# Optimization experiments

Measured on AMD Instinct MI355X. Metric: run time of the kernel, lower is better.

## Reference

```python
import jax, jax.numpy as jnp
import numpy as np

B, S, D, H = 4, 2048, 1024, 4096
EPS = 1e-5

def _layernorm(x, g, b):
    mu = jnp.mean(x, axis=-1, keepdims=True)
    var = jnp.mean(jnp.square(x - mu), axis=-1, keepdims=True)
    return (x - mu) * jax.lax.rsqrt(var + EPS) * g + b

def setup_inputs() -> dict:
    key = jax.random.key(0)
    ks = jax.random.split(key, 8)
    s = lambda d: 1.0 / np.sqrt(d)
    return {
        "x": jax.random.normal(ks[0], (B, S, D), jnp.float32),
        "Wq": jax.random.normal(ks[1], (D, D), jnp.float32) * s(D),
        "bq": jnp.zeros((D,), jnp.float32),
        "Wk": jax.random.normal(ks[2], (D, D), jnp.float32) * s(D),
        "bk": jnp.zeros((D,), jnp.float32),
        "Wv": jax.random.normal(ks[3], (D, D), jnp.float32) * s(D),
        "bv": jnp.zeros((D,), jnp.float32),
        "Wo": jax.random.normal(ks[4], (D, D), jnp.float32) * s(D),
        "bo": jnp.zeros((D,), jnp.float32),
        "g1": jnp.ones((D,), jnp.float32),
        "be1": jnp.zeros((D,), jnp.float32),
        "g2": jnp.ones((D,), jnp.float32),
        "be2": jnp.zeros((D,), jnp.float32),
        "W1": jax.random.normal(ks[5], (D, H), jnp.float32) * s(D),
        "b1": jnp.zeros((H,), jnp.float32),
        "W2": jax.random.normal(ks[6], (H, D), jnp.float32) * s(H),
        "b2": jnp.zeros((D,), jnp.float32),
    }

def reference(x, Wq, bq, Wk, bk, Wv, bv, Wo, bo, g1, be1, g2, be2, W1, b1, W2, b2):
    # pre-norm self-attention + residual
    xn = _layernorm(x, g1, be1)
    q = xn @ Wq + bq            # [B,S,D]
    k = xn @ Wk + bk
    v = xn @ Wv + bv
    scale = 1.0 / jnp.sqrt(jnp.float32(D))
    scores = jnp.einsum("bsd,btd->bst", q, k) * scale  # [B,S,S]
    attn = jax.nn.softmax(scores, axis=-1)
    attn_out = jnp.einsum("bst,btd->bsd", attn, v) @ Wo + bo
    x = x + attn_out
    # pre-norm MLP + residual
    xn2 = _layernorm(x, g2, be2)
    ffn = jax.nn.relu(xn2 @ W1 + b1) @ W2 + b2
    out = x + ffn
    return out, attn
```

## Files before the change

### kernel.cpp

```cpp
#include <hip/hip_runtime.h>
#include <hip/hip_bf16.h>


typedef __bf16 bf16_t;
typedef __bf16 bf16x8 __attribute__((ext_vector_type(8)));
typedef float  f32x4  __attribute__((ext_vector_type(4)));

#define EPI_QKV            0
#define EPI_F32_SCALE      2
#define EPI_BF16           3
#define EPI_F32_BIAS_RES   4
#define EPI_BF16_RELU_BIAS 5

__device__ __forceinline__ void gl_lds16(const bf16_t* g, void* l) {
  __builtin_amdgcn_global_load_lds(
      (const __attribute__((address_space(1))) void*)g,
      (__attribute__((address_space(3))) void*)l, 16, 0, 0);
}

template<int BM, int EPI>
__global__ __launch_bounds__(512, 2)
void gemm8p(const bf16_t* __restrict__ A, const bf16_t* __restrict__ B,
            float* __restrict__ Cf, bf16_t* __restrict__ Cb,
            bf16_t* __restrict__ Cb2, bf16_t* __restrict__ Cb3,
            const float* __restrict__ bias, const float* __restrict__ bias2,
            const float* __restrict__ bias3,
            int M, int N, int K, long sAb, long sBb, long sCb, float scale)
{
  constexpr int BN  = 256;
  constexpr int WTM = BM / 2;
  constexpr int MF  = WTM / 16;
  constexpr int NF  = 4;
  constexpr int LA  = BM / 128;
  constexpr int LB  = 2;
  constexpr int L   = LA + LB;
  constexpr int L0  = 2;
  constexpr int SBUF = (BM + BN) * 64;
  constexpr int W   = 2 * L;
  __shared__ __align__(16) char lds[4 * SBUF];

  const int tid = threadIdx.x;
  const int l   = tid & 63;
  const int w   = tid >> 6;
  const int wm  = w >> 2;
  const int wn  = w & 3;

  const int nx = gridDim.x, ny = gridDim.y;
  const int tot = nx * ny * gridDim.z;
  int id = blockIdx.x + nx * (blockIdx.y + ny * blockIdx.z);
  const int cpx = tot >> 3;
  int s = (id & 7) * cpx + (id >> 3);
  const int bx = s % nx; int rq = s / nx;
  const int by = rq % ny; const int bz = rq / ny;

  const bf16_t* Ab = A + (long)bz * sAb;
  const bf16_t* Bb = B + (long)bz * sBb;
  const int m0 = by * BM, n0 = bx * BN;
  const int NT = K >> 5;

  const int srow = w * 16 + (l >> 2);
  const int scol = ((l & 3) ^ ((l >> 3) & 3)) * 8;
  const bf16_t* srcA[LA]; const bf16_t* srcB[LB];
#pragma unroll
  for (int q = 0; q < LA; ++q) srcA[q] = Ab + (long)(m0 + q * 128 + srow) * K + scol;
#pragma unroll
  for (int q = 0; q < LB; ++q) srcB[q] = Bb + (long)(n0 + q * 128 + srow) * K + scol;
  const int ldsA = w * 1024;
  const int ldsB = BM * 64 + w * 1024;

  const int rA0 = wm * WTM + (l & 15);
  const int rB0 = wn * 64 + (l & 15);
  const int xoff = 16 * ((l >> 4) ^ ((l >> 1) & 3));

  f32x4 acc[MF][NF] = {};
  bf16x8 afr[MF / 2], bfr[NF];

#pragma unroll
  for (int d = 0; d < 3; ++d) {
    char* bufS = lds + d * SBUF;
    const long kst = (long)d * 32;
#pragma unroll
    for (int q = 0; q < LA; ++q) gl_lds16(srcA[q] + kst, bufS + ldsA + q * 8192);
#pragma unroll
    for (int q = 0; q < LB; ++q) gl_lds16(srcB[q] + kst, bufS + ldsB + q * 8192);
  }
  asm volatile("s_waitcnt vmcnt(%0)" :: "n"(W) : "memory");
  __builtin_amdgcn_s_barrier();
  __builtin_amdgcn_sched_barrier(0);

  for (int t = 0; t < NT; ++t) {
    const char* bufR = lds + (t & 3) * SBUF;
    char* bufS = lds + ((t + 3) & 3) * SBUF;
    const int tst = t + 3;
    const long kst = (long)((tst < NT) ? tst : (NT - 1)) * 32;

#pragma unroll
    for (int nf = 0; nf < NF; ++nf)
      bfr[nf] = *(const bf16x8*)(bufR + BM * 64 + (rB0 + nf * 16) * 64 + xoff);
#pragma unroll
    for (int mf = 0; mf < MF / 2; ++mf)
      afr[mf] = *(const bf16x8*)(bufR + (rA0 + mf * 16) * 64 + xoff);
#pragma unroll
    for (int q = 0; q < L0; ++q) {
      if (q < LA) gl_lds16(srcA[q] + kst, bufS + ldsA + q * 8192);
      else        gl_lds16(srcB[q - LA] + kst, bufS + ldsB + (q - LA) * 8192);
    }
    __builtin_amdgcn_s_barrier();
    __builtin_amdgcn_s_setprio(1);
#pragma unroll
    for (int mf = 0; mf < MF / 2; ++mf)
#pragma unroll
      for (int nf = 0; nf < NF; ++nf)
        acc[mf][nf] = __builtin_amdgcn_mfma_f32_16x16x32_bf16(afr[mf], bfr[nf], acc[mf][nf], 0, 0, 0);
    __builtin_amdgcn_s_setprio(0);
    __builtin_amdgcn_s_barrier();

#pragma unroll
    for (int mf = 0; mf < MF / 2; ++mf)
      afr[mf] = *(const bf16x8*)(bufR + (rA0 + (MF / 2 + mf) * 16) * 64 + xoff);
#pragma unroll
    for (int q = L0; q < L; ++q) {
      if (q < LA) gl_lds16(srcA[q] + kst, bufS + ldsA + q * 8192);
      else        gl_lds16(srcB[q - LA] + kst, bufS + ldsB + (q - LA) * 8192);
    }
    __builtin_amdgcn_s_barrier();
    __builtin_amdgcn_s_setprio(1);
#pragma unroll
    for (int mf = 0; mf < MF / 2; ++mf)
#pragma unroll
      for (int nf = 0; nf < NF; ++nf)
        acc[MF / 2 + mf][nf] = __builtin_amdgcn_mfma_f32_16x16x32_bf16(afr[mf], bfr[nf], acc[MF / 2 + mf][nf], 0, 0, 0);
    __builtin_amdgcn_s_setprio(0);
    asm volatile("s_waitcnt vmcnt(%0)" :: "n"(W) : "memory");
    __builtin_amdgcn_s_barrier();
    __builtin_amdgcn_sched_barrier(0);
  }
  asm volatile("s_waitcnt vmcnt(0)" ::: "memory");

  const int colB0 = n0 + wn * 64 + (l & 15);
  const int rowB0 = m0 + wm * WTM + ((l >> 4) << 2);
#pragma unroll
  for (int mi = 0; mi < MF; ++mi) {
#pragma unroll
    for (int ni = 0; ni < NF; ++ni) {
      const int col = colB0 + ni * 16;
#pragma unroll
      for (int j = 0; j < 4; ++j) {
        const int row = rowB0 + mi * 16 + j;
        const float v = acc[mi][ni][j];
        if constexpr (EPI == EPI_F32_SCALE) {
          Cf[sCb * bz + (long)row * N + col] = v * scale;
        } else if constexpr (EPI == EPI_QKV) {
          if (col < 1024)      Cb [(long)row * 1024 + col]        = (bf16_t)(v + bias[col]);
          else if (col < 2048) Cb2[(long)row * 1024 + col - 1024] = (bf16_t)(v + bias2[col - 1024]);
          else                 Cb3[(long)row * 1024 + col - 2048] = (bf16_t)(v + bias3[col - 2048]);
        } else {
          const float u = v + bias[col];
          Cb[(long)row * N + col] = (bf16_t)(u > 0.f ? u : 0.f);
        }
      }
    }
  }
}

template<int EPI>
__global__ __launch_bounds__(512, 1)
void gemm128(const bf16_t* __restrict__ A, const bf16_t* __restrict__ B,
             float* __restrict__ Cf, bf16_t* __restrict__ Cb,
             const float* __restrict__ bias, const float* __restrict__ resid,
             int M, int N, int K, long sAb, long sBb, long sCb)
{
  constexpr int SBUF = 49152;
  __shared__ __align__(16) char lds[3 * SBUF];
  const int tid = threadIdx.x;
  const int l   = tid & 63;
  const int w   = tid >> 6;
  const int wm  = w >> 2, wn = w & 3;

  const int nx = gridDim.x, ny = gridDim.y;
  const int tot = nx * ny * gridDim.z;
  int id = blockIdx.x + nx * (blockIdx.y + ny * blockIdx.z);
  const int cpx = tot >> 3;
  int sid = (id & 7) * cpx + (id >> 3);
  const int bx = sid % nx; int rq = sid / nx;
  const int by = rq % ny; const int bz = rq / ny;

  const bf16_t* Ab = A + (long)bz * sAb;
  const bf16_t* Bb = B + (long)bz * sBb;
  const int m0 = by * 128, n0 = bx * 256;
  const int NT = K >> 6;

  const int scol = ((l & 7) ^ (l >> 3)) * 8;
  const bf16_t* srcA = Ab + (long)(m0 + 16 * w + (l >> 3)) * K + scol;
  const bf16_t* srcB = Bb + (long)(n0 + 32 * w + (l >> 3)) * K + scol;
  const int dA = w * 2048 + l * 16;
  const int dB = 16384 + w * 4096 + l * 16;

  const int rA = wm * 64 + (l & 15);
  const int rB = wn * 64 + (l & 15);
  const int xo = ((l >> 4) ^ (l & 7)) * 16;
  const int aoff = rA * 128 + xo;
  const int boff = 16384 + rB * 128 + xo;

  f32x4 acc[4][4] = {};
  bf16x8 af[4], bv[4];

  {
    char* b0 = lds; char* b1 = lds + SBUF;
#pragma unroll
    for (int q = 0; q < 2; ++q) gl_lds16(srcA + (long)q * 8 * K, b0 + dA + q * 1024);
#pragma unroll
    for (int q = 0; q < 4; ++q) gl_lds16(srcB + (long)q * 8 * K, b0 + dB + q * 1024);
#pragma unroll
    for (int q = 0; q < 2; ++q) gl_lds16(srcA + (long)q * 8 * K + 64, b1 + dA + q * 1024);
#pragma unroll
    for (int q = 0; q < 4; ++q) gl_lds16(srcB + (long)q * 8 * K + 64, b1 + dB + q * 1024);
  }
  asm volatile("s_waitcnt vmcnt(6)" ::: "memory");
  __builtin_amdgcn_s_barrier();
  __builtin_amdgcn_sched_barrier(0);

  int ir = 0, is = 2;
  for (int t = 0; t < NT; ++t) {
    const char* bufR = lds + ir * SBUF;
    char* bufS = lds + is * SBUF;
    const int tst = (t + 2 < NT) ? t + 2 : NT - 1;
    const long kst = (long)tst * 64;

#pragma unroll
    for (int nf = 0; nf < 4; ++nf) bv[nf] = *(const bf16x8*)(bufR + boff + nf * 2048);
#pragma unroll
    for (int mf = 0; mf < 4; ++mf) af[mf] = *(const bf16x8*)(bufR + aoff + mf * 2048);
    gl_lds16(srcA + kst,                 bufS + dA);
    gl_lds16(srcA + (long)8 * K + kst,   bufS + dA + 1024);
    gl_lds16(srcB + kst,                 bufS + dB);
    __builtin_amdgcn_s_barrier();
    __builtin_amdgcn_s_setprio(1);
#pragma unroll
    for (int mf = 0; mf < 4; ++mf)
#pragma unroll
      for (int nf = 0; nf < 4; ++nf)
        acc[mf][nf] = __builtin_amdgcn_mfma_f32_16x16x32_bf16(af[mf], bv[nf], acc[mf][nf], 0, 0, 0);
    __builtin_amdgcn_s_setprio(0);
    __builtin_amdgcn_s_barrier();

#pragma unroll
    for (int nf = 0; nf < 4; ++nf) bv[nf] = *(const bf16x8*)(bufR + ((boff + nf * 2048) ^ 64));
#pragma unroll
    for (int mf = 0; mf < 4; ++mf) af[mf] = *(const bf16x8*)(bufR + ((aoff + mf * 2048) ^ 64));
    gl_lds16(srcB + (long)8 * K + kst,   bufS + dB + 1024);
    gl_lds16(srcB + (long)16 * K + kst,  bufS + dB + 2048);
    gl_lds16(srcB + (long)24 * K + kst,  bufS + dB + 3072);
    __builtin_amdgcn_s_barrier();
    __builtin_amdgcn_s_setprio(1);
#pragma unroll
    for (int mf = 0; mf < 4; ++mf)
#pragma unroll
      for (int nf = 0; nf < 4; ++nf)
        acc[mf][nf] = __builtin_amdgcn_mfma_f32_16x16x32_bf16(af[mf], bv[nf], acc[mf][nf], 0, 0, 0);
    __builtin_amdgcn_s_setprio(0);
    asm volatile("s_waitcnt vmcnt(6)" ::: "memory");
    __builtin_amdgcn_s_barrier();
    __builtin_amdgcn_sched_barrier(0);
    ir = (ir == 2) ? 0 : ir + 1;
    is = (is == 2) ? 0 : is + 1;
  }
  asm volatile("s_waitcnt vmcnt(0)" ::: "memory");

  const int colB0 = n0 + wn * 64 + (l & 15);
  const int rowB0 = m0 + wm * 64 + ((l >> 4) << 2);
#pragma unroll
  for (int mi = 0; mi < 4; ++mi) {
#pragma unroll
    for (int ni = 0; ni < 4; ++ni) {
      const int col = colB0 + ni * 16;
#pragma unroll
      for (int j = 0; j < 4; ++j) {
        const int row = rowB0 + mi * 16 + j;
        const float v = acc[mi][ni][j];
        if constexpr (EPI == EPI_BF16) {
          Cb[sCb * bz + (long)row * N + col] = (bf16_t)v;
        } else {
          Cf[(long)row * N + col] = v + bias[col] + resid[(long)row * N + col];
        }
      }
    }
  }
}

__global__ __launch_bounds__(256)
void transpose_bf(const bf16_t* __restrict__ V, bf16_t* __restrict__ VT)
{
  __shared__ __align__(16) bf16_t t[64][72];
  const int b = blockIdx.z;
  const int t0 = blockIdx.y * 64, d0 = blockIdx.x * 64;
  const int r = threadIdx.x >> 3;
  const int c = (threadIdx.x & 7) * 8;
  const bf16_t* src = V + ((long)b * 2048 + t0) * 1024 + d0;
#pragma unroll
  for (int h = 0; h < 2; ++h)
    *(bf16x8*)&t[r + 32 * h][c] = *(const bf16x8*)(src + (long)(r + 32 * h) * 1024 + c);
  __syncthreads();
  bf16_t* dst = VT + ((long)b * 1024 + d0) * 2048 + t0;
#pragma unroll
  for (int h = 0; h < 2; ++h) {
    const int d = r + 32 * h;
    bf16x8 o;
#pragma unroll
    for (int j = 0; j < 8; ++j) o[j] = t[c + j][d];
    *(bf16x8*)(dst + (long)d * 2048 + c) = o;
  }
}

__global__ __launch_bounds__(256)
void ln_kernel(const float* __restrict__ x, const float* __restrict__ g,
               const float* __restrict__ be, bf16_t* __restrict__ out)
{
  const long row = blockIdx.x;
  const float4 v = *(const float4*)(x + row * 1024 + threadIdx.x * 4);
  float s  = v.x + v.y + v.z + v.w;
  float s2 = v.x * v.x + v.y * v.y + v.z * v.z + v.w * v.w;
  __shared__ float red[10];
  const int lane = threadIdx.x & 63, w = threadIdx.x >> 6;
#pragma unroll
  for (int off = 32; off; off >>= 1) {
    s  += __shfl_down(s, off);
    s2 += __shfl_down(s2, off);
  }
  if (lane == 0) { red[w] = s; red[4 + w] = s2; }
  __syncthreads();
  if (threadIdx.x == 0) {
    const float ts = red[0] + red[1] + red[2] + red[3];
    const float t2 = red[4] + red[5] + red[6] + red[7];
    const float mu = ts * (1.f / 1024.f);
    const float var = t2 * (1.f / 1024.f) - mu * mu;
    red[8] = mu;
    red[9] = rsqrtf(var + 1e-5f);
  }
  __syncthreads();
  const float mu = red[8], rinv = red[9];
  const int c = threadIdx.x * 4;
  const float4 gv = *(const float4*)(g + c);
  const float4 bvv = *(const float4*)(be + c);
  bf16_t* o = out + row * 1024 + c;
  o[0] = (bf16_t)((v.x - mu) * rinv * gv.x + bvv.x);
  o[1] = (bf16_t)((v.y - mu) * rinv * gv.y + bvv.y);
  o[2] = (bf16_t)((v.z - mu) * rinv * gv.z + bvv.z);
  o[3] = (bf16_t)((v.w - mu) * rinv * gv.w + bvv.w);
}

__global__ __launch_bounds__(256)
void softmax_kernel(float* __restrict__ sc, bf16_t* __restrict__ ab)
{
  const long row = blockIdx.x;
  float* sr = sc + row * 2048;
  const int t0 = threadIdx.x * 8;
  const float4 a = *(const float4*)(sr + t0);
  const float4 b = *(const float4*)(sr + t0 + 4);
  float mx = fmaxf(fmaxf(fmaxf(a.x, a.y), fmaxf(a.z, a.w)),
                   fmaxf(fmaxf(b.x, b.y), fmaxf(b.z, b.w)));
  __shared__ float red[4];
  __shared__ float bc[2];
  const int lane = threadIdx.x & 63, w = threadIdx.x >> 6;
#pragma unroll
  for (int off = 32; off; off >>= 1) mx = fmaxf(mx, __shfl_down(mx, off));
  if (lane == 0) red[w] = mx;
  __syncthreads();
  if (threadIdx.x == 0) bc[0] = fmaxf(fmaxf(red[0], red[1]), fmaxf(red[2], red[3]));
  __syncthreads();
  const float m = bc[0];
  float e[8];
  e[0] = __expf(a.x - m); e[1] = __expf(a.y - m); e[2] = __expf(a.z - m); e[3] = __expf(a.w - m);
  e[4] = __expf(b.x - m); e[5] = __expf(b.y - m); e[6] = __expf(b.z - m); e[7] = __expf(b.w - m);
  float s = e[0] + e[1] + e[2] + e[3] + e[4] + e[5] + e[6] + e[7];
#pragma unroll
  for (int off = 32; off; off >>= 1) s += __shfl_down(s, off);
  __syncthreads();
  if (lane == 0) red[w] = s;
  __syncthreads();
  if (threadIdx.x == 0) bc[1] = 1.f / (red[0] + red[1] + red[2] + red[3]);
  __syncthreads();
  const float inv = bc[1];
  float4 oa, ob;
  oa.x = e[0] * inv; oa.y = e[1] * inv; oa.z = e[2] * inv; oa.w = e[3] * inv;
  ob.x = e[4] * inv; ob.y = e[5] * inv; ob.z = e[6] * inv; ob.w = e[7] * inv;
  *(float4*)(sr + t0)     = oa;
  *(float4*)(sr + t0 + 4) = ob;
  bf16x8 o8;
  o8[0] = (bf16_t)oa.x; o8[1] = (bf16_t)oa.y; o8[2] = (bf16_t)oa.z; o8[3] = (bf16_t)oa.w;
  o8[4] = (bf16_t)ob.x; o8[5] = (bf16_t)ob.y; o8[6] = (bf16_t)ob.z; o8[7] = (bf16_t)ob.w;
  *(bf16x8*)(ab + row * 2048 + t0) = o8;
}

__global__ __launch_bounds__(256)
void transpose_cvt(const float* __restrict__ W, bf16_t* __restrict__ WT, int R, int C)
{
  __shared__ float t[32][33];
  const int c0 = blockIdx.x * 32, r0 = blockIdx.y * 32;
  const int tx = threadIdx.x & 31, ty = threadIdx.x >> 5;
#pragma unroll
  for (int i = 0; i < 32; i += 8)
    t[ty + i][tx] = W[(long)(r0 + ty + i) * C + c0 + tx];
  __syncthreads();
#pragma unroll
  for (int i = 0; i < 32; i += 8)
    WT[(long)(c0 + ty + i) * R + r0 + tx] = (bf16_t)t[tx][ty + i];
}

extern "C" void kernel_launch(void* const* d_in, const int* in_sizes, int n_in,
                              void* d_out, int out_size, void* d_ws, size_t ws_size,
                              hipStream_t stream)
{
  const float* x   = (const float*)d_in[0];
  const float* Wq  = (const float*)d_in[1];
  const float* bq  = (const float*)d_in[2];
  const float* Wk  = (const float*)d_in[3];
  const float* bk  = (const float*)d_in[4];
  const float* Wv  = (const float*)d_in[5];
  const float* bv  = (const float*)d_in[6];
  const float* Wo  = (const float*)d_in[7];
  const float* bo  = (const float*)d_in[8];
  const float* g1  = (const float*)d_in[9];
  const float* be1 = (const float*)d_in[10];
  const float* g2  = (const float*)d_in[11];
  const float* be2 = (const float*)d_in[12];
  const float* W1  = (const float*)d_in[13];
  const float* b1  = (const float*)d_in[14];
  const float* W2  = (const float*)d_in[15];
  const float* b2  = (const float*)d_in[16];

  float* out   = (float*)d_out;
  float* attnF = out + 8192L * 1024;
  bf16_t* vB   = (bf16_t*)attnF;

  char* ws = (char*)d_ws;
  const size_t MB = 1024 * 1024;
  bf16_t* WqkvT = (bf16_t*)(ws + 0 * MB);
  bf16_t* WoT   = (bf16_t*)(ws + 6 * MB);
  bf16_t* W1T   = (bf16_t*)(ws + 8 * MB);
  bf16_t* W2T   = (bf16_t*)(ws + 16 * MB);
  bf16_t* xn    = (bf16_t*)(ws + 24 * MB);
  bf16_t* qB    = (bf16_t*)(ws + 40 * MB);
  bf16_t* kB    = (bf16_t*)(ws + 56 * MB);
  bf16_t* vT    = (bf16_t*)(ws + 72 * MB);
  bf16_t* atB   = (bf16_t*)(ws + 88 * MB);
  float*  x2    = (float* )(ws + 120 * MB);
  bf16_t* hB    = (bf16_t*)(ws + 56 * MB);

  transpose_cvt<<<dim3(32, 32),  256, 0, stream>>>(Wq, WqkvT,                1024, 1024);
  transpose_cvt<<<dim3(32, 32),  256, 0, stream>>>(Wk, WqkvT + 1024L * 1024, 1024, 1024);
  transpose_cvt<<<dim3(32, 32),  256, 0, stream>>>(Wv, WqkvT + 2048L * 1024, 1024, 1024);
  transpose_cvt<<<dim3(32, 32),  256, 0, stream>>>(Wo, WoT, 1024, 1024);
  transpose_cvt<<<dim3(128, 32), 256, 0, stream>>>(W1, W1T, 1024, 4096);
  transpose_cvt<<<dim3(32, 128), 256, 0, stream>>>(W2, W2T, 4096, 1024);

  ln_kernel<<<8192, 256, 0, stream>>>(x, g1, be1, xn);

  gemm8p<256, EPI_QKV><<<dim3(12, 32, 1), 512, 0, stream>>>(
      xn, WqkvT, nullptr, qB, kB, vB, bq, bk, bv,
      8192, 3072, 1024, 0, 0, 0, 1.f);

  transpose_bf<<<dim3(16, 32, 4), 256, 0, stream>>>(vB, vT);

  gemm8p<256, EPI_F32_SCALE><<<dim3(8, 8, 4), 512, 0, stream>>>(
      qB, kB, attnF, nullptr, nullptr, nullptr, nullptr, nullptr, nullptr,
      2048, 2048, 1024, 2048L * 1024, 2048L * 1024, 2048L * 2048, 0.03125f);

  softmax_kernel<<<8192, 256, 0, stream>>>(attnF, atB);

  gemm128<EPI_BF16><<<dim3(4, 16, 4), 512, 0, stream>>>(
      atB, vT, nullptr, qB, nullptr, nullptr,
      2048, 1024, 2048, 2048L * 2048, 1024L * 2048, 2048L * 1024);

  gemm128<EPI_F32_BIAS_RES><<<dim3(4, 64, 1), 512, 0, stream>>>(
      qB, WoT, x2, nullptr, bo, x,
      8192, 1024, 1024, 0, 0, 0);

  ln_kernel<<<8192, 256, 0, stream>>>(x2, g2, be2, xn);

  gemm8p<256, EPI_BF16_RELU_BIAS><<<dim3(16, 32, 1), 512, 0, stream>>>(
      xn, W1T, nullptr, hB, nullptr, nullptr, b1, nullptr, nullptr,
      8192, 4096, 1024, 0, 0, 0, 1.f);
  gemm128<EPI_F32_BIAS_RES><<<dim3(4, 64, 1), 512, 0, stream>>>(
      hB, W2T, out, nullptr, b2, x2,
      8192, 1024, 4096, 0, 0, 0);
}
```

Measured before the change: 428.1 us.

## Store attention scores as bf16 and add a dedicated 128x256 QKV GEMM

The scores GEMM now writes scaled logits as bf16 into the bf16 attention buffer instead of fp32 into the fp32 attention output. Softmax reads those bf16 logits, then writes the fp32 probabilities and overwrites the bf16 copy in place. This cuts the scores write and the softmax read traffic roughly in half. The QKV projection moves to a new simpler double-buffered 128x256 tile kernel with K-step 32 and 2 blocks per CU, for better occupancy. The cost is that logits are rounded to bf16 before softmax, which reduces accuracy of the returned attention matrix.

```diff
diff --git a/kernel.cpp b/kernel.cpp
--- a/kernel.cpp
+++ b/kernel.cpp
@@ -7,7 +7,7 @@
 typedef float  f32x4  __attribute__((ext_vector_type(4)));
 
 #define EPI_QKV            0
-#define EPI_F32_SCALE      2
+#define EPI_BF16_SCALE     1
 #define EPI_BF16           3
 #define EPI_F32_BIAS_RES   4
 #define EPI_BF16_RELU_BIAS 5
@@ -22,9 +22,7 @@
 __global__ __launch_bounds__(512, 2)
 void gemm8p(const bf16_t* __restrict__ A, const bf16_t* __restrict__ B,
             float* __restrict__ Cf, bf16_t* __restrict__ Cb,
-            bf16_t* __restrict__ Cb2, bf16_t* __restrict__ Cb3,
-            const float* __restrict__ bias, const float* __restrict__ bias2,
-            const float* __restrict__ bias3,
+            const float* __restrict__ bias,
             int M, int N, int K, long sAb, long sBb, long sCb, float scale)
 {
   constexpr int BN  = 256;
@@ -148,12 +146,8 @@
       for (int j = 0; j < 4; ++j) {
         const int row = rowB0 + mi * 16 + j;
         const float v = acc[mi][ni][j];
-        if constexpr (EPI == EPI_F32_SCALE) {
-          Cf[sCb * bz + (long)row * N + col] = v * scale;
-        } else if constexpr (EPI == EPI_QKV) {
-          if (col < 1024)      Cb [(long)row * 1024 + col]        = (bf16_t)(v + bias[col]);
-          else if (col < 2048) Cb2[(long)row * 1024 + col - 1024] = (bf16_t)(v + bias2[col - 1024]);
-          else                 Cb3[(long)row * 1024 + col - 2048] = (bf16_t)(v + bias3[col - 2048]);
+        if constexpr (EPI == EPI_BF16_SCALE) {
+          Cb[sCb * bz + (long)row * N + col] = (bf16_t)(v * scale);
         } else {
           const float u = v + bias[col];
           Cb[(long)row * N + col] = (bf16_t)(u > 0.f ? u : 0.f);
@@ -288,6 +282,98 @@
   }
 }
 
+__global__ __launch_bounds__(512, 2)
+void gemm128_32(const bf16_t* __restrict__ A, const bf16_t* __restrict__ B,
+                bf16_t* __restrict__ Cb, bf16_t* __restrict__ Cb2,
+                bf16_t* __restrict__ Cb3,
+                const float* __restrict__ bias, const float* __restrict__ bias2,
+                const float* __restrict__ bias3, int M, int N, int K)
+{
+  constexpr int SBUF = 24576;
+  __shared__ __align__(16) char lds[2 * SBUF];
+  const int tid = threadIdx.x;
+  const int l   = tid & 63;
+  const int w   = tid >> 6;
+  const int wm  = w >> 2, wn = w & 3;
+
+  const int nx = gridDim.x, ny = gridDim.y;
+  const int tot = nx * ny;
+  int id = blockIdx.x + nx * blockIdx.y;
+  const int cpx = tot >> 3;
+  int sid = (id & 7) * cpx + (id >> 3);
+  const int bx = sid % nx;
+  const int by = sid / nx;
+
+  const int m0 = by * 128, n0 = bx * 256;
+  const int NT = K >> 5;
+
+  const int srow = (l >> 2);
+  const int scol = ((l & 3) ^ ((l >> 3) & 3)) * 8;
+  const bf16_t* srcA = A + (long)(m0 + w * 16 + srow) * K + scol;
+  const bf16_t* srcB0 = B + (long)(n0 + w * 32 + srow) * K + scol;
+  const bf16_t* srcB1 = srcB0 + (long)16 * K;
+  const int dA = w * 1024 + l * 16;
+  const int dB = 8192 + w * 2048 + l * 16;
+
+  const int rA = wm * 64 + (l & 15);
+  const int rB = wn * 64 + (l & 15);
+  const int xoff = 16 * ((l >> 4) ^ ((l >> 1) & 3));
+  const int aoff = rA * 64 + xoff;
+  const int boff = 8192 + rB * 64 + xoff;
+
+  f32x4 acc[4][4] = {};
+  bf16x8 af[4], bv[4];
+
+  gl_lds16(srcA, lds + dA);
+  gl_lds16(srcB0, lds + dB);
+  gl_lds16(srcB1, lds + dB + 1024);
+  asm volatile("s_waitcnt vmcnt(0)" ::: "memory");
+  __builtin_amdgcn_s_barrier();
+  __builtin_amdgcn_sched_barrier(0);
+
+  for (int t = 0; t < NT; ++t) {
+    const char* bufR = lds + (t & 1) * SBUF;
+    char* bufS = lds + ((t + 1) & 1) * SBUF;
+    const long kst = (long)((t + 1 < NT) ? t + 1 : NT - 1) * 32;
+
+#pragma unroll
+    for (int nf = 0; nf < 4; ++nf) bv[nf] = *(const bf16x8*)(bufR + boff + nf * 1024);
+#pragma unroll
+    for (int mf = 0; mf < 4; ++mf) af[mf] = *(const bf16x8*)(bufR + aoff + mf * 1024);
+    gl_lds16(srcA + kst, bufS + dA);
+    gl_lds16(srcB0 + kst, bufS + dB);
+    gl_lds16(srcB1 + kst, bufS + dB + 1024);
+    __builtin_amdgcn_s_setprio(1);
+#pragma unroll
+    for (int mf = 0; mf < 4; ++mf)
+#pragma unroll
+      for (int nf = 0; nf < 4; ++nf)
+        acc[mf][nf] = __builtin_amdgcn_mfma_f32_16x16x32_bf16(af[mf], bv[nf], acc[mf][nf], 0, 0, 0);
+    __builtin_amdgcn_s_setprio(0);
+    asm volatile("s_waitcnt vmcnt(0)" ::: "memory");
+    __builtin_amdgcn_s_barrier();
+    __builtin_amdgcn_sched_barrier(0);
+  }
+
+  const int colB0 = n0 + wn * 64 + (l & 15);
+  const int rowB0 = m0 + wm * 64 + ((l >> 4) << 2);
+#pragma unroll
+  for (int mi = 0; mi < 4; ++mi) {
+#pragma unroll
+    for (int ni = 0; ni < 4; ++ni) {
+      const int col = colB0 + ni * 16;
+#pragma unroll
+      for (int j = 0; j < 4; ++j) {
+        const int row = rowB0 + mi * 16 + j;
+        const float v = acc[mi][ni][j];
+        if (col < 1024)      Cb [(long)row * 1024 + col]        = (bf16_t)(v + bias[col]);
+        else if (col < 2048) Cb2[(long)row * 1024 + col - 1024] = (bf16_t)(v + bias2[col - 1024]);
+        else                 Cb3[(long)row * 1024 + col - 2048] = (bf16_t)(v + bias3[col - 2048]);
+      }
+    }
+  }
+}
+
 __global__ __launch_bounds__(256)
 void transpose_bf(const bf16_t* __restrict__ V, bf16_t* __restrict__ VT)
 {
@@ -353,12 +439,13 @@
 void softmax_kernel(float* __restrict__ sc, bf16_t* __restrict__ ab)
 {
   const long row = blockIdx.x;
-  float* sr = sc + row * 2048;
   const int t0 = threadIdx.x * 8;
-  const float4 a = *(const float4*)(sr + t0);
-  const float4 b = *(const float4*)(sr + t0 + 4);
-  float mx = fmaxf(fmaxf(fmaxf(a.x, a.y), fmaxf(a.z, a.w)),
-                   fmaxf(fmaxf(b.x, b.y), fmaxf(b.z, b.w)));
+  const bf16x8 v8 = *(const bf16x8*)(ab + row * 2048 + t0);
+  float e[8];
+#pragma unroll
+  for (int j = 0; j < 8; ++j) e[j] = (float)v8[j];
+  float mx = fmaxf(fmaxf(fmaxf(e[0], e[1]), fmaxf(e[2], e[3])),
+                   fmaxf(fmaxf(e[4], e[5]), fmaxf(e[6], e[7])));
   __shared__ float red[4];
   __shared__ float bc[2];
   const int lane = threadIdx.x & 63, w = threadIdx.x >> 6;
@@ -369,10 +456,9 @@
   if (threadIdx.x == 0) bc[0] = fmaxf(fmaxf(red[0], red[1]), fmaxf(red[2], red[3]));
   __syncthreads();
   const float m = bc[0];
-  float e[8];
-  e[0] = __expf(a.x - m); e[1] = __expf(a.y - m); e[2] = __expf(a.z - m); e[3] = __expf(a.w - m);
-  e[4] = __expf(b.x - m); e[5] = __expf(b.y - m); e[6] = __expf(b.z - m); e[7] = __expf(b.w - m);
-  float s = e[0] + e[1] + e[2] + e[3] + e[4] + e[5] + e[6] + e[7];
+  float s = 0.f;
+#pragma unroll
+  for (int j = 0; j < 8; ++j) { e[j] = __expf(e[j] - m); s += e[j]; }
 #pragma unroll
   for (int off = 32; off; off >>= 1) s += __shfl_down(s, off);
   __syncthreads();
@@ -384,8 +470,8 @@
   float4 oa, ob;
   oa.x = e[0] * inv; oa.y = e[1] * inv; oa.z = e[2] * inv; oa.w = e[3] * inv;
   ob.x = e[4] * inv; ob.y = e[5] * inv; ob.z = e[6] * inv; ob.w = e[7] * inv;
-  *(float4*)(sr + t0)     = oa;
-  *(float4*)(sr + t0 + 4) = ob;
+  *(float4*)(sc + row * 2048 + t0)     = oa;
+  *(float4*)(sc + row * 2048 + t0 + 4) = ob;
   bf16x8 o8;
   o8[0] = (bf16_t)oa.x; o8[1] = (bf16_t)oa.y; o8[2] = (bf16_t)oa.z; o8[3] = (bf16_t)oa.w;
   o8[4] = (bf16_t)ob.x; o8[5] = (bf16_t)ob.y; o8[6] = (bf16_t)ob.z; o8[7] = (bf16_t)ob.w;
@@ -456,14 +542,13 @@
 
   ln_kernel<<<8192, 256, 0, stream>>>(x, g1, be1, xn);
 
-  gemm8p<256, EPI_QKV><<<dim3(12, 32, 1), 512, 0, stream>>>(
-      xn, WqkvT, nullptr, qB, kB, vB, bq, bk, bv,
-      8192, 3072, 1024, 0, 0, 0, 1.f);
+  gemm128_32<<<dim3(12, 64), 512, 0, stream>>>(
+      xn, WqkvT, qB, kB, vB, bq, bk, bv, 8192, 3072, 1024);
 
   transpose_bf<<<dim3(16, 32, 4), 256, 0, stream>>>(vB, vT);
 
-  gemm8p<256, EPI_F32_SCALE><<<dim3(8, 8, 4), 512, 0, stream>>>(
-      qB, kB, attnF, nullptr, nullptr, nullptr, nullptr, nullptr, nullptr,
+  gemm8p<256, EPI_BF16_SCALE><<<dim3(8, 8, 4), 512, 0, stream>>>(
+      qB, kB, nullptr, atB, nullptr,
       2048, 2048, 1024, 2048L * 1024, 2048L * 1024, 2048L * 2048, 0.03125f);
 
   softmax_kernel<<<8192, 256, 0, stream>>>(attnF, atB);
@@ -479,7 +564,7 @@
   ln_kernel<<<8192, 256, 0, stream>>>(x2, g2, be2, xn);
 
   gemm8p<256, EPI_BF16_RELU_BIAS><<<dim3(16, 32, 1), 512, 0, stream>>>(
-      xn, W1T, nullptr, hB, nullptr, nullptr, b1, nullptr, nullptr,
+      xn, W1T, nullptr, hB, b1,
       8192, 4096, 1024, 0, 0, 0, 1.f);
   gemm128<EPI_F32_BIAS_RES><<<dim3(4, 64, 1), 512, 0, stream>>>(
       hB, W2T, out, nullptr, b2, x2,
```

Measured after the change: 401.4 us. 1.07x faster.
